# Kernel tuning notes

Hardware: AMD Instinct MI355X
Metric: run time of the kernel (lower is better)

The kernel has to match this reference:

```python
import jax, jax.numpy as jnp
import numpy as np

B, H, S, D = 4, 16, 4096, 64

def setup_inputs() -> dict:
    key = jax.random.key(0)
    kq, kk, kv = jax.random.split(key, 3)
    q = jax.random.normal(kq, (B, H, S, D), dtype=jnp.float32)
    k = jax.random.normal(kk, (B, H, S, D), dtype=jnp.float32)
    v = jax.random.normal(kv, (B, H, S, D), dtype=jnp.float32)
    return {"q": q, "k": k, "v": v}

def reference(q, k, v):
    # Original: (q @ k^T) @ v with score [B,H,S,S].
    # Mathematically identical reassociation: q @ (k^T @ v),
    # state kv has shape [B,H,D,D] -> avoids the SxS intermediate.
    kv = jnp.einsum('bhsd,bhse->bhde', k, v)  # [B,H,D,D]
    out = jnp.einsum('bhsd,bhde->bhse', q, kv)  # [B,H,S,D]
    return out
```

## Files before the change

kernel.cpp:

```cpp
#include <hip/hip_runtime.h>

#define BH  64
#define SEQ 4096
#define DH  64
#define NCHUNK 32
#define CROWS  (SEQ / NCHUNK)
#define NT     (CROWS / 32)

typedef __attribute__((ext_vector_type(8))) short bf16x8v;
typedef __attribute__((ext_vector_type(4))) float f32x4v;

__device__ __forceinline__ short f2bf(float x) {
  unsigned u = __float_as_uint(x);
  return (short)((u + 0x7FFFu + ((u >> 16) & 1u)) >> 16);
}

__device__ __forceinline__ void gload_lds16(const float* g, float* l) {
  __builtin_amdgcn_global_load_lds(
      (const __attribute__((address_space(1))) void*)g,
      (__attribute__((address_space(3))) void*)l, 16, 0, 0);
}

__global__ __launch_bounds__(64) void kv_partial_kernel(
    const float* __restrict__ k, const float* __restrict__ v,
    float* __restrict__ partial) {
  const int l  = threadIdx.x;
  const int bh = blockIdx.x >> 5;
  const int chunk = blockIdx.x & (NCHUNK - 1);
  const int lg = l >> 4;
  const int ln = l & 15;

  const float* kb = k + (size_t)bh * SEQ * DH + (size_t)chunk * CROWS * DH;
  const float* vb = v + (size_t)bh * SEQ * DH + (size_t)chunk * CROWS * DH;

  __shared__ float smem[8192];

  f32x4v acc[4][4];
#pragma unroll
  for (int m = 0; m < 4; ++m)
#pragma unroll
    for (int n = 0; n < 4; ++n) acc[m][n] = (f32x4v){0.f, 0.f, 0.f, 0.f};

  auto STAGE = [&](int tt) {
    const int buf = tt & 1;
    const float* kt = kb + (size_t)tt * 2048;
    const float* vt = vb + (size_t)tt * 2048;
    float* kd = smem + buf * 2048;
    float* vd = smem + 4096 + buf * 2048;
#pragma unroll
    for (int i = 0; i < 8; ++i) {
      const int so = (i * 4 + lg) * 64 + ((ln * 4) ^ (((i >> 1) & 3) << 4));
      gload_lds16(kt + so, kd + i * 256);
      gload_lds16(vt + so, vd + i * 256);
    }
  };

  auto COMPUTE = [&](int tt) {
    const float* ks = smem + (tt & 1) * 2048;
    const float* vs = smem + 4096 + (tt & 1) * 2048;
    bf16x8v a[4], b[4];
#pragma unroll
    for (int c = 0; c < 4; ++c) {
#pragma unroll
      for (int j = 0; j < 8; ++j) {
        const int addr = (lg * 8 + j) * 64 + ((c * 16 + ln) ^ (lg << 4));
        a[c][j] = f2bf(ks[addr]);
        b[c][j] = f2bf(vs[addr]);
      }
    }
#pragma unroll
    for (int m = 0; m < 4; ++m)
#pragma unroll
      for (int n = 0; n < 4; ++n)
        acc[m][n] = __builtin_amdgcn_mfma_f32_16x16x32_bf16(
            a[m], b[n], acc[m][n], 0, 0, 0);
  };

  STAGE(0);
  STAGE(1);
#pragma unroll
  for (int tt = 0; tt < NT; ++tt) {
    if (tt + 1 < NT) {
      asm volatile("s_waitcnt vmcnt(16)" ::: "memory");
    } else {
      asm volatile("s_waitcnt vmcnt(0)" ::: "memory");
    }
    __builtin_amdgcn_sched_barrier(0);
    COMPUTE(tt);
    __builtin_amdgcn_sched_barrier(0);
    if (tt + 2 < NT) STAGE(tt + 2);
  }

  float* pb = partial + (size_t)blockIdx.x * (DH * DH);
#pragma unroll
  for (int m = 0; m < 4; ++m)
#pragma unroll
    for (int n = 0; n < 4; ++n)
#pragma unroll
      for (int r = 0; r < 4; ++r)
        pb[(m * 16 + lg * 4 + r) * 64 + n * 16 + ln] = acc[m][n][r];
}

__global__ __launch_bounds__(256) void kv_reduce_kernel(
    const float* __restrict__ partial, float* __restrict__ kvf) {
  const int gid = blockIdx.x * 256 + threadIdx.x;
  const int bh = gid >> 10;
  const int idx = gid & 1023;
  float4 s = {0.f, 0.f, 0.f, 0.f};
  for (int c = 0; c < NCHUNK; ++c) {
    const float4* p = (const float4*)(partial + ((size_t)bh * NCHUNK + c) * (DH * DH));
    float4 x = p[idx];
    s.x += x.x; s.y += x.y; s.z += x.z; s.w += x.w;
  }
  ((float4*)kvf)[gid] = s;
}

__global__ __launch_bounds__(256) void out_kernel(
    const float* __restrict__ q, const float* __restrict__ kvf,
    float* __restrict__ out) {
  const int t = threadIdx.x;
  const int bh = blockIdx.x >> 6;
  const int rb = blockIdx.x & 63;
  const int row = rb * 64 + (t >> 2);
  const int c0 = (t & 3) * 16;

  __shared__ float kv_lds[64 * 64];

  const float4* gkv4 = (const float4*)(kvf + (size_t)bh * (DH * DH));
  float4* kv4 = (float4*)kv_lds;
#pragma unroll
  for (int j = 0; j < 4; ++j) kv4[t + j * 256] = gkv4[t + j * 256];

  const float* qrow = q + (size_t)bh * SEQ * DH + (size_t)row * DH;
  float4 qv[16];
#pragma unroll
  for (int i = 0; i < 16; ++i) qv[i] = *(const float4*)&qrow[i * 4];

  __syncthreads();

  float acc[16];
#pragma unroll
  for (int j = 0; j < 16; ++j) acc[j] = 0.f;

#pragma unroll
  for (int dc = 0; dc < 16; ++dc) {
    float qs[4] = {qv[dc].x, qv[dc].y, qv[dc].z, qv[dc].w};
#pragma unroll
    for (int dd = 0; dd < 4; ++dd) {
      const float* kr = &kv_lds[(dc * 4 + dd) * 64 + c0];
      float4 k0 = *(const float4*)&kr[0];
      float4 k1 = *(const float4*)&kr[4];
      float4 k2 = *(const float4*)&kr[8];
      float4 k3 = *(const float4*)&kr[12];
      const float qsv = qs[dd];
      acc[0]  += qsv * k0.x; acc[1]  += qsv * k0.y;
      acc[2]  += qsv * k0.z; acc[3]  += qsv * k0.w;
      acc[4]  += qsv * k1.x; acc[5]  += qsv * k1.y;
      acc[6]  += qsv * k1.z; acc[7]  += qsv * k1.w;
      acc[8]  += qsv * k2.x; acc[9]  += qsv * k2.y;
      acc[10] += qsv * k2.z; acc[11] += qsv * k2.w;
      acc[12] += qsv * k3.x; acc[13] += qsv * k3.y;
      acc[14] += qsv * k3.z; acc[15] += qsv * k3.w;
    }
  }

  float* ob = out + (size_t)bh * SEQ * DH + (size_t)row * DH + c0;
#pragma unroll
  for (int j = 0; j < 4; ++j) {
    float4 w = {acc[4 * j + 0], acc[4 * j + 1], acc[4 * j + 2], acc[4 * j + 3]};
    *(float4*)&ob[4 * j] = w;
  }
}

extern "C" void kernel_launch(void* const* d_in, const int* in_sizes, int n_in,
                              void* d_out, int out_size, void* d_ws, size_t ws_size,
                              hipStream_t stream) {
  const float* q = (const float*)d_in[0];
  const float* k = (const float*)d_in[1];
  const float* v = (const float*)d_in[2];
  float* out = (float*)d_out;

  float* kvf = (float*)d_ws;
  float* partial = kvf + (size_t)BH * DH * DH;

  hipLaunchKernelGGL(kv_partial_kernel, dim3(BH * NCHUNK), dim3(64), 0, stream,
                     k, v, partial);
  hipLaunchKernelGGL(kv_reduce_kernel, dim3(256), dim3(256), 0, stream,
                     partial, kvf);
  hipLaunchKernelGGL(out_kernel, dim3(BH * 64), dim3(256), 0, stream,
                     q, kvf, out);
}
```

Baseline: 82.92 us.

## Split kv partial chunk across four waves with direct register loads and LDS reduction

The kv_partial kernel now runs 256 threads per block. Each of the four waves loads its own 32-row slice of K and V straight from global memory into registers, converts to bf16 and issues one round of MFMAs, in place of a single wave looping over four double-buffered LDS tiles. The four per-wave accumulators are then summed with a two-step reduction through shared memory before wave 0 writes the partial. This gives more waves per chunk to hide memory latency, at the cost of uncoalesced scalar loads (each lane reads strided floats), extra syncthreads and LDS traffic.

```diff
diff --git a/kernel.cpp b/kernel.cpp
--- a/kernel.cpp
+++ b/kernel.cpp
@@ -5,7 +5,6 @@
 #define DH  64
 #define NCHUNK 32
 #define CROWS  (SEQ / NCHUNK)
-#define NT     (CROWS / 32)
 
 typedef __attribute__((ext_vector_type(8))) short bf16x8v;
 typedef __attribute__((ext_vector_type(4))) float f32x4v;
@@ -15,90 +14,101 @@
   return (short)((u + 0x7FFFu + ((u >> 16) & 1u)) >> 16);
 }
 
-__device__ __forceinline__ void gload_lds16(const float* g, float* l) {
-  __builtin_amdgcn_global_load_lds(
-      (const __attribute__((address_space(1))) void*)g,
-      (__attribute__((address_space(3))) void*)l, 16, 0, 0);
-}
-
-__global__ __launch_bounds__(64) void kv_partial_kernel(
+__global__ __launch_bounds__(256) void kv_partial_kernel(
     const float* __restrict__ k, const float* __restrict__ v,
     float* __restrict__ partial) {
-  const int l  = threadIdx.x;
+  const int t = threadIdx.x;
   const int bh = blockIdx.x >> 5;
   const int chunk = blockIdx.x & (NCHUNK - 1);
+  const int l  = t & 63;
+  const int w  = t >> 6;
   const int lg = l >> 4;
   const int ln = l & 15;
 
-  const float* kb = k + (size_t)bh * SEQ * DH + (size_t)chunk * CROWS * DH;
-  const float* vb = v + (size_t)bh * SEQ * DH + (size_t)chunk * CROWS * DH;
+  const size_t rowbase = (size_t)bh * SEQ * DH + ((size_t)chunk * CROWS + w * 32) * DH;
+  const float* kb = k + rowbase;
+  const float* vb = v + rowbase;
 
   __shared__ float smem[8192];
 
+  float kf[32], vf[32];
+#pragma unroll
+  for (int j = 0; j < 8; ++j) {
+    const float* kr = kb + (size_t)(lg * 8 + j) * DH;
+    const float* vr = vb + (size_t)(lg * 8 + j) * DH;
+#pragma unroll
+    for (int m = 0; m < 4; ++m) {
+      kf[m * 8 + j] = kr[m * 16 + ln];
+      vf[m * 8 + j] = vr[m * 16 + ln];
+    }
+  }
+
+  bf16x8v a[4], b[4];
+#pragma unroll
+  for (int m = 0; m < 4; ++m)
+#pragma unroll
+    for (int j = 0; j < 8; ++j) {
+      a[m][j] = f2bf(kf[m * 8 + j]);
+      b[m][j] = f2bf(vf[m * 8 + j]);
+    }
+
   f32x4v acc[4][4];
 #pragma unroll
   for (int m = 0; m < 4; ++m)
 #pragma unroll
-    for (int n = 0; n < 4; ++n) acc[m][n] = (f32x4v){0.f, 0.f, 0.f, 0.f};
-
-  auto STAGE = [&](int tt) {
-    const int buf = tt & 1;
-    const float* kt = kb + (size_t)tt * 2048;
-    const float* vt = vb + (size_t)tt * 2048;
-    float* kd = smem + buf * 2048;
-    float* vd = smem + 4096 + buf * 2048;
-#pragma unroll
-    for (int i = 0; i < 8; ++i) {
-      const int so = (i * 4 + lg) * 64 + ((ln * 4) ^ (((i >> 1) & 3) << 4));
-      gload_lds16(kt + so, kd + i * 256);
-      gload_lds16(vt + so, vd + i * 256);
-    }
-  };
-
-  auto COMPUTE = [&](int tt) {
-    const float* ks = smem + (tt & 1) * 2048;
-    const float* vs = smem + 4096 + (tt & 1) * 2048;
-    bf16x8v a[4], b[4];
-#pragma unroll
-    for (int c = 0; c < 4; ++c) {
-#pragma unroll
-      for (int j = 0; j < 8; ++j) {
-        const int addr = (lg * 8 + j) * 64 + ((c * 16 + ln) ^ (lg << 4));
-        a[c][j] = f2bf(ks[addr]);
-        b[c][j] = f2bf(vs[addr]);
-      }
-    }
-#pragma unroll
-    for (int m = 0; m < 4; ++m)
-#pragma unroll
-      for (int n = 0; n < 4; ++n)
-        acc[m][n] = __builtin_amdgcn_mfma_f32_16x16x32_bf16(
-            a[m], b[n], acc[m][n], 0, 0, 0);
-  };
-
-  STAGE(0);
-  STAGE(1);
-#pragma unroll
-  for (int tt = 0; tt < NT; ++tt) {
-    if (tt + 1 < NT) {
-      asm volatile("s_waitcnt vmcnt(16)" ::: "memory");
-    } else {
-      asm volatile("s_waitcnt vmcnt(0)" ::: "memory");
-    }
-    __builtin_amdgcn_sched_barrier(0);
-    COMPUTE(tt);
-    __builtin_amdgcn_sched_barrier(0);
-    if (tt + 2 < NT) STAGE(tt + 2);
-  }
-
-  float* pb = partial + (size_t)blockIdx.x * (DH * DH);
-#pragma unroll
-  for (int m = 0; m < 4; ++m)
-#pragma unroll
-    for (int n = 0; n < 4; ++n)
-#pragma unroll
-      for (int r = 0; r < 4; ++r)
-        pb[(m * 16 + lg * 4 + r) * 64 + n * 16 + ln] = acc[m][n][r];
+    for (int n = 0; n < 4; ++n) {
+      acc[m][n] = (f32x4v){0.f, 0.f, 0.f, 0.f};
+      acc[m][n] = __builtin_amdgcn_mfma_f32_16x16x32_bf16(
+          a[m], b[n], acc[m][n], 0, 0, 0);
+    }
+
+  if (w >= 2) {
+    float* reg = smem + (w - 2) * 4096;
+#pragma unroll
+    for (int m = 0; m < 4; ++m)
+#pragma unroll
+      for (int n = 0; n < 4; ++n) {
+        float4 x = {acc[m][n][0], acc[m][n][1], acc[m][n][2], acc[m][n][3]};
+        *(float4*)&reg[(m * 4 + n) * 256 + l * 4] = x;
+      }
+  }
+  __syncthreads();
+  if (w < 2) {
+    const float* reg = smem + w * 4096;
+#pragma unroll
+    for (int m = 0; m < 4; ++m)
+#pragma unroll
+      for (int n = 0; n < 4; ++n) {
+        float4 x = *(const float4*)&reg[(m * 4 + n) * 256 + l * 4];
+        acc[m][n][0] += x.x; acc[m][n][1] += x.y;
+        acc[m][n][2] += x.z; acc[m][n][3] += x.w;
+      }
+  }
+  __syncthreads();
+  if (w == 1) {
+#pragma unroll
+    for (int m = 0; m < 4; ++m)
+#pragma unroll
+      for (int n = 0; n < 4; ++n) {
+        float4 x = {acc[m][n][0], acc[m][n][1], acc[m][n][2], acc[m][n][3]};
+        *(float4*)&smem[(m * 4 + n) * 256 + l * 4] = x;
+      }
+  }
+  __syncthreads();
+  if (w == 0) {
+    float* pb = partial + (size_t)blockIdx.x * (DH * DH);
+#pragma unroll
+    for (int m = 0; m < 4; ++m)
+#pragma unroll
+      for (int n = 0; n < 4; ++n) {
+        float4 x = *(const float4*)&smem[(m * 4 + n) * 256 + l * 4];
+        acc[m][n][0] += x.x; acc[m][n][1] += x.y;
+        acc[m][n][2] += x.z; acc[m][n][3] += x.w;
+#pragma unroll
+        for (int r = 0; r < 4; ++r)
+          pb[(m * 16 + lg * 4 + r) * 64 + n * 16 + ln] = acc[m][n][r];
+      }
+  }
 }
 
 __global__ __launch_bounds__(256) void kv_reduce_kernel(
@@ -183,7 +193,7 @@
   float* kvf = (float*)d_ws;
   float* partial = kvf + (size_t)BH * DH * DH;
 
-  hipLaunchKernelGGL(kv_partial_kernel, dim3(BH * NCHUNK), dim3(64), 0, stream,
+  hipLaunchKernelGGL(kv_partial_kernel, dim3(BH * NCHUNK), dim3(256), 0, stream,
                      k, v, partial);
   hipLaunchKernelGGL(kv_reduce_kernel, dim3(256), dim3(256), 0, stream,
                      partial, kvf);
```

New measurement: 83.23 us. About the same (+0.4%).
